# Optimization experiments

Hardware: AMD Instinct MI355X
Metric: run time of the kernel (lower is better)

Reference implementation:

```python
import jax, jax.numpy as jnp
import numpy as np

FEA, DK, H = 512, 64, 8
B, L = 4, 2048
EPS = 1e-5


def _layernorm(x, g, b):
    mu = jnp.mean(x, axis=-1, keepdims=True)
    var = jnp.mean(jnp.square(x - mu), axis=-1, keepdims=True)
    return (x - mu) * jax.lax.rsqrt(var + EPS) * g + b


def setup_inputs() -> dict:
    key = jax.random.key(0)
    ks = jax.random.split(key, 12)
    d = {
        'qx': jax.random.normal(ks[0], (B, L, FEA), jnp.float32),
        'kx': jax.random.normal(ks[1], (B, L, FEA), jnp.float32),
        'vx': jax.random.normal(ks[2], (B, L, FEA), jnp.float32),
        'maskPAD': jax.random.randint(ks[3], (B, L, L), 0, 2, jnp.int32),
        # attention projections (stored as [in, out]); biases zero-init as in module
        'wq': jax.random.normal(ks[4], (FEA, DK * H), jnp.float32) * 0.02,
        'bq': jnp.zeros((DK * H,), jnp.float32),
        'wk': jax.random.normal(ks[5], (FEA, DK * H), jnp.float32) * 0.02,
        'bk': jnp.zeros((DK * H,), jnp.float32),
        'wv': jax.random.normal(ks[6], (FEA, DK * H), jnp.float32) * 0.02,
        'bv': jnp.zeros((DK * H,), jnp.float32),
        'wo': jax.random.normal(ks[7], (DK * H, FEA), jnp.float32) * 0.02,
        'bo': jnp.zeros((FEA,), jnp.float32),
        # FFN
        'w1': jax.random.normal(ks[8], (FEA, 4 * FEA), jnp.float32) * 0.02,
        'b1': jnp.zeros((4 * FEA,), jnp.float32),
        'w2': jax.random.normal(ks[9], (4 * FEA, FEA), jnp.float32) * 0.02,
        'b2': jnp.zeros((FEA,), jnp.float32),
        # layer norms
        'ln1_g': jnp.ones((FEA,), jnp.float32),
        'ln1_b': jnp.zeros((FEA,), jnp.float32),
        'ln2_g': jnp.ones((FEA,), jnp.float32),
        'ln2_b': jnp.zeros((FEA,), jnp.float32),
    }
    return d


def reference(qx, kx, vx, maskPAD, wq, bq, wk, bk, wv, bv, wo, bo,
              w1, b1, w2, b2, ln1_g, ln1_b, ln2_g, ln2_b):
    b, l, _ = qx.shape
    # project and split heads: [B, H, L, DK]
    q = (qx @ wq + bq).reshape(b, l, H, DK).transpose(0, 2, 1, 3)
    k = (kx @ wk + bk).reshape(b, l, H, DK).transpose(0, 2, 1, 3)
    v = (vx @ wv + bv).reshape(b, l, H, DK).transpose(0, 2, 1, 3)
    scores = jnp.einsum('bhqd,bhkd->bhqk', q, k) / np.sqrt(DK)  # [B,H,L,L]
    mask = (maskPAD == 0)[:, None, :, :]
    scores = jnp.where(mask, jnp.float32(-2 ** 15 + 1), scores)
    alpha = jax.nn.softmax(scores, axis=-1)
    z = jnp.einsum('bhqk,bhkd->bhqd', alpha, v)  # [B,H,L,DK]
    z = z.transpose(0, 2, 1, 3).reshape(b, l, H * DK)
    z = z @ wo + bo
    # post-LN FFN block (dropout = identity at inference)
    zn = _layernorm(vx + z, ln1_g, ln1_b)
    ffn = jax.nn.gelu(zn @ w1 + b1, approximate=False) @ w2 + b2
    return _layernorm(zn + ffn, ln2_g, ln2_b)
```

## Files before the change

kernel.cpp:

```cpp
#include <hip/hip_runtime.h>
#include <cstdint>


typedef __bf16 bf16;
typedef __bf16 bf16x8 __attribute__((ext_vector_type(8)));
typedef __bf16 bf16x2 __attribute__((ext_vector_type(2)));
typedef float floatx4 __attribute__((ext_vector_type(4)));
typedef unsigned uint2v __attribute__((ext_vector_type(2)));

__device__ __forceinline__ floatx4 mfma_bf16(bf16x8 a, bf16x8 b, floatx4 c) {
  return __builtin_amdgcn_mfma_f32_16x16x32_bf16(a, b, c, 0, 0, 0);
}

__device__ __forceinline__ void load_lds_16(const void* g, void* l) {
  auto gp = reinterpret_cast<const void __attribute__((address_space(1)))*>(
      reinterpret_cast<uintptr_t>(g));
  auto lp = reinterpret_cast<void __attribute__((address_space(3)))*>(
      (unsigned int)reinterpret_cast<uintptr_t>(l));
  __builtin_amdgcn_global_load_lds(gp, lp, 16, 0, 0);
}

__device__ __forceinline__ unsigned pack2(float a, float b) {
  bf16x2 p;
  p[0] = (bf16)a;
  p[1] = (bf16)b;
  return __builtin_bit_cast(unsigned, p);
}

__device__ __forceinline__ float gelu_f(float x) {
  float t = 0.7978845608f * (x + 0.044715f * x * x * x);
  float e = __builtin_amdgcn_exp2f(t * 2.885390082f);
  float th = 1.0f - 2.0f * __builtin_amdgcn_rcpf(e + 1.0f);
  return 0.5f * x * (1.0f + th);
}

#define PLANE128 2064
#define PLANE64 1040

__global__ void __launch_bounds__(256) transpose4_k(const float* __restrict__ w0,
                                                    const float* __restrict__ w1,
                                                    const float* __restrict__ w2,
                                                    const float* __restrict__ w3,
                                                    bf16* __restrict__ o0,
                                                    bf16* __restrict__ o1,
                                                    bf16* __restrict__ o2,
                                                    bf16* __restrict__ o3) {
  const float* in = (blockIdx.z == 0) ? w0 : (blockIdx.z == 1) ? w1
                    : (blockIdx.z == 2) ? w2 : w3;
  bf16* out = (blockIdx.z == 0) ? o0 : (blockIdx.z == 1) ? o1
              : (blockIdx.z == 2) ? o2 : o3;
  __shared__ float tile[32][33];
  int m0 = blockIdx.x * 32, k0 = blockIdx.y * 32;
  int tx = threadIdx.x, ty = threadIdx.y;
  for (int i = ty; i < 32; i += 8)
    tile[i][tx] = in[(size_t)(k0 + i) * 512 + m0 + tx];
  __syncthreads();
  for (int i = ty; i < 32; i += 8)
    out[(size_t)(m0 + i) * 512 + k0 + tx] = (bf16)tile[tx][i];
}

__global__ void __launch_bounds__(256) transpose_k(const float* __restrict__ in,
                                                   bf16* __restrict__ out,
                                                   int K, int M) {
  __shared__ float tile[32][33];
  int m0 = blockIdx.x * 32, k0 = blockIdx.y * 32;
  int tx = threadIdx.x, ty = threadIdx.y;
  for (int i = ty; i < 32; i += 8)
    tile[i][tx] = in[(size_t)(k0 + i) * M + m0 + tx];
  __syncthreads();
  for (int i = ty; i < 32; i += 8)
    out[(size_t)(m0 + i) * K + k0 + tx] = (bf16)tile[tx][i];
}

__global__ void __launch_bounds__(256) maskbits_k(const int* __restrict__ m,
                                                  unsigned long long* __restrict__ out) {
  int w = blockIdx.x * 4 + (threadIdx.x >> 6);
  int lane = threadIdx.x & 63;
  int v = m[(size_t)w * 64 + lane];
  unsigned long long b = __ballot(v != 0);
  if (lane == 0) out[w] = b;
}

template <int EPI>
__device__ __forceinline__ void epi_store(void* Cout, int n, int m, int M,
                                          float val) {
  if constexpr (EPI == 1) {
    int bb = n >> 11, l = n & 2047, hh = m >> 6, d = m & 63;
    ((bf16*)Cout)[((size_t)((bb * 8 + hh) * 2048 + l)) * 64 + d] = (bf16)val;
  } else if constexpr (EPI == 2) {
    int bb = n >> 11, l = n & 2047, hh = m >> 6, d = m & 63;
    ((bf16*)Cout)[((size_t)((bb * 8 + hh) * 64 + d)) * 2048 + l] = (bf16)val;
  } else if constexpr (EPI == 3) {
    ((bf16*)Cout)[(size_t)n * M + m] = (bf16)gelu_f(val);
  } else if constexpr (EPI == 4) {
    ((float*)Cout)[(size_t)n * M + m] = val;
  } else {
    ((float*)Cout)[(size_t)n * M + m] += val;
  }
}

template <int EPI, bool TALL>
__global__ void __launch_bounds__(256) gemm_bt(const bf16* __restrict__ A,
                                               const bf16* __restrict__ Bt,
                                               const float* __restrict__ bias,
                                               void* __restrict__ Cout,
                                               int M, int K, int lda, int ldb) {
  __shared__ __attribute__((aligned(16))) char As[8 * PLANE128];
  __shared__ __attribute__((aligned(16))) char Bs[TALL ? 8 * PLANE64 : 8 * PLANE128];
  int tid = threadIdx.x, wave = tid >> 6, lane = tid & 63;
  int lrow = lane & 15, quad = lane >> 4;
  int n0 = blockIdx.y * 128;
  int m0 = blockIdx.x * (TALL ? 64 : 128);
  int wr = wave >> 1, wc = wave & 1;
  floatx4 zero4 = {0.f, 0.f, 0.f, 0.f};
  constexpr int NI = TALL ? 2 : 4;
  floatx4 acc[NI][4];
#pragma unroll
  for (int i = 0; i < NI; ++i)
#pragma unroll
    for (int j = 0; j < 4; ++j) acc[i][j] = zero4;
  for (int k0 = 0; k0 < K; k0 += 64) {
    __syncthreads();
#pragma unroll
    for (int h = 0; h < 2; ++h) {
      int p = wave + 4 * h;
#pragma unroll
      for (int j = 0; j < 2; ++j) {
        int row = j * 64 + lane;
        load_lds_16(A + (size_t)(n0 + row) * lda + k0 + p * 8,
                    As + p * PLANE128 + j * 1024 + lane * 16);
      }
      if constexpr (TALL) {
        load_lds_16(Bt + (size_t)(m0 + lane) * ldb + k0 + p * 8,
                    Bs + p * PLANE64 + lane * 16);
      } else {
#pragma unroll
        for (int j = 0; j < 2; ++j) {
          int row = j * 64 + lane;
          load_lds_16(Bt + (size_t)(m0 + row) * ldb + k0 + p * 8,
                      Bs + p * PLANE128 + j * 1024 + lane * 16);
        }
      }
    }
    __syncthreads();
#pragma unroll
    for (int h = 0; h < 2; ++h) {
      int pb = h * 4 + quad;
      bf16x8 af[NI], bfr[4];
#pragma unroll
      for (int i = 0; i < NI; ++i) {
        int row = (TALL ? wave * 32 : wr * 64) + i * 16 + lrow;
        af[i] = *(const bf16x8*)(As + pb * PLANE128 + row * 16);
      }
#pragma unroll
      for (int j = 0; j < 4; ++j) {
        if constexpr (TALL)
          bfr[j] = *(const bf16x8*)(Bs + pb * PLANE64 + (j * 16 + lrow) * 16);
        else
          bfr[j] = *(const bf16x8*)(Bs + pb * PLANE128 +
                                    (wc * 64 + j * 16 + lrow) * 16);
      }
#pragma unroll
      for (int i = 0; i < NI; ++i)
#pragma unroll
        for (int j = 0; j < 4; ++j)
          acc[i][j] = mfma_bf16(af[i], bfr[j], acc[i][j]);
    }
  }
  float bv[4];
#pragma unroll
  for (int j = 0; j < 4; ++j) {
    int m = m0 + (TALL ? 0 : wc * 64) + j * 16 + lrow;
    bv[j] = (EPI == 5) ? 0.f : bias[m];
  }
#pragma unroll
  for (int i = 0; i < NI; ++i)
#pragma unroll
    for (int j = 0; j < 4; ++j)
#pragma unroll
      for (int r = 0; r < 4; ++r) {
        int n = n0 + (TALL ? wave * 32 : wr * 64) + i * 16 + quad * 4 + r;
        int m = m0 + (TALL ? 0 : wc * 64) + j * 16 + lrow;
        epi_store<EPI>(Cout, n, m, M, acc[i][j][r] + bv[j]);
      }
}

__global__ void __launch_bounds__(256) qkv_k(const float* __restrict__ qx,
                                             const float* __restrict__ kx,
                                             const float* __restrict__ vx,
                                             const bf16* __restrict__ wqT,
                                             const bf16* __restrict__ wkT,
                                             const bf16* __restrict__ wvT,
                                             const float* __restrict__ bq,
                                             const float* __restrict__ bk,
                                             const float* __restrict__ bv_,
                                             bf16* __restrict__ qh,
                                             bf16* __restrict__ kh,
                                             bf16* __restrict__ vt) {
  __shared__ __attribute__((aligned(16))) char As[8 * PLANE128];
  __shared__ __attribute__((aligned(16))) char Bs[8 * PLANE128];
  int tid = threadIdx.x, wave = tid >> 6, lane = tid & 63;
  int lrow = lane & 15, quad = lane >> 4;
  int seg = blockIdx.y >> 6;
  int n0 = (blockIdx.y & 63) * 128, m0 = blockIdx.x * 128;
  const float* Af = (seg == 0) ? qx : (seg == 1) ? kx : vx;
  const bf16* Bt = (seg == 0) ? wqT : (seg == 1) ? wkT : wvT;
  const float* bias = (seg == 0) ? bq : (seg == 1) ? bk : bv_;
  bf16* out = (seg == 0) ? qh : (seg == 1) ? kh : vt;
  int wr = wave >> 1, wc = wave & 1;
  floatx4 zero4 = {0.f, 0.f, 0.f, 0.f};
  floatx4 acc[4][4];
#pragma unroll
  for (int i = 0; i < 4; ++i)
#pragma unroll
    for (int j = 0; j < 4; ++j) acc[i][j] = zero4;
  int arow = tid >> 2, ap = tid & 3;
  for (int k0 = 0; k0 < 512; k0 += 64) {
    bf16x8 a[4];
#pragma unroll
    for (int u = 0; u < 4; ++u) {
      int row = arow + (u & 1) * 64, p = ap + (u >> 1) * 4;
      const float* src = Af + (size_t)(n0 + row) * 512 + k0 + p * 8;
      float4 x0 = *(const float4*)src;
      float4 x1 = *(const float4*)(src + 4);
      a[u][0] = (bf16)x0.x; a[u][1] = (bf16)x0.y; a[u][2] = (bf16)x0.z;
      a[u][3] = (bf16)x0.w; a[u][4] = (bf16)x1.x; a[u][5] = (bf16)x1.y;
      a[u][6] = (bf16)x1.z; a[u][7] = (bf16)x1.w;
    }
    __syncthreads();
#pragma unroll
    for (int u = 0; u < 4; ++u) {
      int row = arow + (u & 1) * 64, p = ap + (u >> 1) * 4;
      *(bf16x8*)(As + p * PLANE128 + row * 16) = a[u];
    }
#pragma unroll
    for (int h = 0; h < 2; ++h) {
      int p = wave + 4 * h;
#pragma unroll
      for (int j = 0; j < 2; ++j) {
        int row = j * 64 + lane;
        load_lds_16(Bt + (size_t)(m0 + row) * 512 + k0 + p * 8,
                    Bs + p * PLANE128 + j * 1024 + lane * 16);
      }
    }
    __syncthreads();
#pragma unroll
    for (int h = 0; h < 2; ++h) {
      int pb = h * 4 + quad;
      bf16x8 af[4], bfr[4];
#pragma unroll
      for (int t = 0; t < 4; ++t) {
        af[t] = *(const bf16x8*)(As + pb * PLANE128 + (wr * 64 + t * 16 + lrow) * 16);
        bfr[t] = *(const bf16x8*)(Bs + pb * PLANE128 + (wc * 64 + t * 16 + lrow) * 16);
      }
#pragma unroll
      for (int i = 0; i < 4; ++i)
#pragma unroll
        for (int j = 0; j < 4; ++j) acc[i][j] = mfma_bf16(af[i], bfr[j], acc[i][j]);
    }
  }
  float bvv[4];
#pragma unroll
  for (int j = 0; j < 4; ++j) bvv[j] = bias[m0 + wc * 64 + j * 16 + lrow];
#pragma unroll
  for (int i = 0; i < 4; ++i)
#pragma unroll
    for (int j = 0; j < 4; ++j)
#pragma unroll
      for (int r = 0; r < 4; ++r) {
        int n = n0 + wr * 64 + i * 16 + quad * 4 + r;
        int m = m0 + wc * 64 + j * 16 + lrow;
        float val = acc[i][j][r] + bvv[j];
        int bb = n >> 11, l = n & 2047, hh = m >> 6, d = m & 63;
        if (seg == 2)
          out[((size_t)((bb * 8 + hh) * 64 + d)) * 2048 + l] = (bf16)val;
        else
          out[((size_t)((bb * 8 + hh) * 2048 + l)) * 64 + d] = (bf16)val;
      }
}

__global__ void __launch_bounds__(256) attn_k(const bf16* __restrict__ Qh,
                                              const bf16* __restrict__ Kh,
                                              const bf16* __restrict__ Vt,
                                              const unsigned long long* __restrict__ MB,
                                              bf16* __restrict__ Z) {
  __shared__ __attribute__((aligned(16))) char Ks[2][8 * PLANE64];
  __shared__ __attribute__((aligned(16))) char Vs[2][8 * PLANE64];
  int qt = blockIdx.x, h = blockIdx.y, b = blockIdx.z;
  int tid = threadIdx.x, wave = tid >> 6, lane = tid & 63;
  int lrow = lane & 15, quad = lane >> 4;
  int q0 = qt * 128;
  size_t headbase = (size_t)(b * 8 + h) * 2048 * 64;

  bf16x8 qf[2][2];
#pragma unroll
  for (int u = 0; u < 2; ++u) {
    const bf16* Qp =
        Qh + headbase + (size_t)(q0 + wave * 32 + u * 16 + lrow) * 64 + quad * 8;
    qf[u][0] = *(const bf16x8*)Qp;
    qf[u][1] = *(const bf16x8*)(Qp + 32);
  }

  floatx4 zero4 = {0.f, 0.f, 0.f, 0.f};
  floatx4 o_acc[2][4], acc_l[2];
#pragma unroll
  for (int u = 0; u < 2; ++u) {
    acc_l[u] = zero4;
#pragma unroll
    for (int dt = 0; dt < 4; ++dt) o_acc[u][dt] = zero4;
  }
  bf16x8 ones;
#pragma unroll
  for (int j = 0; j < 8; ++j) ones[j] = (bf16)1.0f;

  const bf16* Vg = Vt + headbase;
  const bf16* Kg0 = Kh + headbase;
  const uint2* MB0 =
      (const uint2*)(MB + ((size_t)b * 2048 + q0 + wave * 32 + lrow) * 32);
  const float C = 0.1803368801f;
  int sh = quad * 4;

  auto stage = [&](int buf, int kt) {
    int kk = kt * 64;
    const bf16* Kg = Kg0 + (size_t)kk * 64;
#pragma unroll
    for (int j = 0; j < 2; ++j) {
      int p = wave * 2 + j;
      load_lds_16(Kg + (size_t)lane * 64 + p * 8,
                  Ks[buf] + p * PLANE64 + lane * 16);
      load_lds_16(Vg + (size_t)lane * 2048 + kk + p * 8,
                  Vs[buf] + p * PLANE64 + lane * 16);
    }
  };

  stage(0, 0);
  uint2 mwc[2] = {MB0[0], MB0[512]};

  for (int kt = 0; kt < 32; ++kt) {
    int cur = kt & 1;
    __syncthreads();
    uint2 mwn[2];
    if (kt < 31) {
      stage(cur ^ 1, kt + 1);
      mwn[0] = MB0[kt + 1];
      mwn[1] = MB0[512 + kt + 1];
    }
    const char* Kc = Ks[cur];
    const char* Vc = Vs[cur];
    unsigned S[2][4][2];
#pragma unroll
    for (int nt = 0; nt < 4; ++nt) {
      int R = nt * 16 + lrow;
      bf16x8 k0f = *(const bf16x8*)(Kc + quad * PLANE64 + R * 16);
      bf16x8 k1f = *(const bf16x8*)(Kc + (quad + 4) * PLANE64 + R * 16);
#pragma unroll
      for (int u = 0; u < 2; ++u) {
        floatx4 aa = zero4;
        aa = mfma_bf16(k0f, qf[u][0], aa);
        aa = mfma_bf16(k1f, qf[u][1], aa);
        floatx4 sc = aa * C;
        unsigned wn = ((nt & 2) ? mwc[u].y : mwc[u].x) >> ((nt & 1) * 16 + sh);
        float e[4];
#pragma unroll
        for (int r = 0; r < 4; ++r)
          e[r] = (wn & (1u << r)) ? __builtin_amdgcn_exp2f(sc[r]) : 0.f;
        S[u][nt][0] = pack2(e[0], e[1]);
        S[u][nt][1] = pack2(e[2], e[3]);
      }
    }
    bf16x8 v0[4], v1[4];
#pragma unroll
    for (int dt = 0; dt < 4; ++dt) {
      int R = dt * 16 + lrow;
      v0[dt] = *(const bf16x8*)(Vc + quad * PLANE64 + R * 16);
      v1[dt] = *(const bf16x8*)(Vc + (quad + 4) * PLANE64 + R * 16);
    }
#pragma unroll
    for (int u = 0; u < 2; ++u) {
      union { unsigned w[4]; bf16x8 v; } pf[2];
#pragma unroll
      for (int half = 0; half < 2; ++half)
#pragma unroll
        for (int pr = 0; pr < 2; ++pr) {
          uint2v a = __builtin_amdgcn_permlane32_swap(
              S[u][half * 2][pr], S[u][half * 2 + 1][pr], false, false);
          uint2v c = __builtin_amdgcn_permlane16_swap(a[0], a[1], false, false);
          pf[half].w[pr] = c[0];
          pf[half].w[pr + 2] = c[1];
        }
      bf16x8 pf0 = pf[0].v, pf1 = pf[1].v;
      __builtin_amdgcn_s_setprio(1);
      acc_l[u] = mfma_bf16(pf0, ones, acc_l[u]);
      acc_l[u] = mfma_bf16(pf1, ones, acc_l[u]);
#pragma unroll
      for (int dt = 0; dt < 4; ++dt) {
        o_acc[u][dt] = mfma_bf16(pf0, v0[dt], o_acc[u][dt]);
        o_acc[u][dt] = mfma_bf16(pf1, v1[dt], o_acc[u][dt]);
      }
      __builtin_amdgcn_s_setprio(0);
    }
    if (kt < 31) { mwc[0] = mwn[0]; mwc[1] = mwn[1]; }
  }
#pragma unroll
  for (int u = 0; u < 2; ++u) {
    float lr[4];
#pragma unroll
    for (int r = 0; r < 4; ++r) lr[r] = 1.0f / acc_l[u][r];
#pragma unroll
    for (int dt = 0; dt < 4; ++dt)
#pragma unroll
      for (int r = 0; r < 4; ++r) {
        int qrow = q0 + wave * 32 + u * 16 + quad * 4 + r;
        int d = dt * 16 + lrow;
        Z[((size_t)(b * 2048 + qrow)) * 512 + h * 64 + d] =
            (bf16)(o_acc[u][dt][r] * lr[r]);
      }
  }
}

template <bool A_BF16, bool OUT_BF16>
__global__ void __launch_bounds__(256) ln_k(const void* __restrict__ a_,
                                            const float* __restrict__ s,
                                            const float* __restrict__ g,
                                            const float* __restrict__ bta,
                                            void* __restrict__ out_) {
  int row = blockIdx.x * 4 + (threadIdx.x >> 6);
  int lane = threadIdx.x & 63;
  size_t base = (size_t)row * 512 + lane * 8;
  float x[8];
  float4 sa = *(const float4*)(s + base);
  float4 sb = *(const float4*)(s + base + 4);
  if constexpr (A_BF16) {
    bf16x8 av = *(const bf16x8*)((const bf16*)a_ + base);
    x[0] = (float)av[0] + sa.x; x[1] = (float)av[1] + sa.y;
    x[2] = (float)av[2] + sa.z; x[3] = (float)av[3] + sa.w;
    x[4] = (float)av[4] + sb.x; x[5] = (float)av[5] + sb.y;
    x[6] = (float)av[6] + sb.z; x[7] = (float)av[7] + sb.w;
  } else {
    float4 a0 = *(const float4*)((const float*)a_ + base);
    float4 a1 = *(const float4*)((const float*)a_ + base + 4);
    x[0] = a0.x + sa.x; x[1] = a0.y + sa.y; x[2] = a0.z + sa.z; x[3] = a0.w + sa.w;
    x[4] = a1.x + sb.x; x[5] = a1.y + sb.y; x[6] = a1.z + sb.z; x[7] = a1.w + sb.w;
  }
  float sum = 0.f;
#pragma unroll
  for (int i = 0; i < 8; ++i) sum += x[i];
#pragma unroll
  for (int off = 1; off < 64; off <<= 1) sum += __shfl_xor(sum, off, 64);
  float mu = sum * (1.0f / 512.0f);
  float vs = 0.f;
#pragma unroll
  for (int i = 0; i < 8; ++i) { float d = x[i] - mu; vs += d * d; }
#pragma unroll
  for (int off = 1; off < 64; off <<= 1) vs += __shfl_xor(vs, off, 64);
  float rstd = rsqrtf(vs * (1.0f / 512.0f) + 1e-5f);
  float4 g0 = *(const float4*)(g + lane * 8);
  float4 g1 = *(const float4*)(g + lane * 8 + 4);
  float4 b0 = *(const float4*)(bta + lane * 8);
  float4 b1 = *(const float4*)(bta + lane * 8 + 4);
  float gg[8] = {g0.x, g0.y, g0.z, g0.w, g1.x, g1.y, g1.z, g1.w};
  float bb[8] = {b0.x, b0.y, b0.z, b0.w, b1.x, b1.y, b1.z, b1.w};
  if constexpr (OUT_BF16) {
    bf16x8 o;
#pragma unroll
    for (int i = 0; i < 8; ++i)
      o[i] = (bf16)((x[i] - mu) * rstd * gg[i] + bb[i]);
    *(bf16x8*)((bf16*)out_ + base) = o;
  } else {
    float4 o0, o1;
    o0.x = (x[0] - mu) * rstd * gg[0] + bb[0];
    o0.y = (x[1] - mu) * rstd * gg[1] + bb[1];
    o0.z = (x[2] - mu) * rstd * gg[2] + bb[2];
    o0.w = (x[3] - mu) * rstd * gg[3] + bb[3];
    o1.x = (x[4] - mu) * rstd * gg[4] + bb[4];
    o1.y = (x[5] - mu) * rstd * gg[5] + bb[5];
    o1.z = (x[6] - mu) * rstd * gg[6] + bb[6];
    o1.w = (x[7] - mu) * rstd * gg[7] + bb[7];
    *(float4*)((float*)out_ + base) = o0;
    *(float4*)((float*)out_ + base + 4) = o1;
  }
}

extern "C" void kernel_launch(void* const* d_in, const int* in_sizes, int n_in,
                              void* d_out, int out_size, void* d_ws, size_t ws_size,
                              hipStream_t stream) {
  const float* qx = (const float*)d_in[0];
  const float* kx = (const float*)d_in[1];
  const float* vx = (const float*)d_in[2];
  const int* maskPAD = (const int*)d_in[3];
  const float* wq = (const float*)d_in[4];
  const float* bq = (const float*)d_in[5];
  const float* wk = (const float*)d_in[6];
  const float* bk = (const float*)d_in[7];
  const float* wv = (const float*)d_in[8];
  const float* bv = (const float*)d_in[9];
  const float* wo = (const float*)d_in[10];
  const float* bo = (const float*)d_in[11];
  const float* w1 = (const float*)d_in[12];
  const float* b1 = (const float*)d_in[13];
  const float* w2 = (const float*)d_in[14];
  const float* b2 = (const float*)d_in[15];
  const float* g1 = (const float*)d_in[16];
  const float* be1 = (const float*)d_in[17];
  const float* g2 = (const float*)d_in[18];
  const float* be2 = (const float*)d_in[19];

  char* w = (char*)d_ws;
  size_t off = 0;
  auto alloc = [&](size_t bytes) {
    void* p = w + off;
    off += (bytes + 255) & ~(size_t)255;
    return p;
  };
  bf16* wqT = (bf16*)alloc(512 * 512 * 2);
  bf16* wkT = (bf16*)alloc(512 * 512 * 2);
  bf16* wvT = (bf16*)alloc(512 * 512 * 2);
  bf16* woT = (bf16*)alloc(512 * 512 * 2);
  bf16* w1T = (bf16*)alloc(2048 * 512 * 2);
  bf16* w2T = (bf16*)alloc(512 * 2048 * 2);
  unsigned long long* mbits = (unsigned long long*)alloc((size_t)4 * 2048 * 32 * 8);
  bf16* qh = (bf16*)alloc((size_t)8192 * 512 * 2);
  bf16* kh = (bf16*)alloc((size_t)8192 * 512 * 2);
  bf16* vt = (bf16*)alloc((size_t)8192 * 512 * 2);
  bf16* z = (bf16*)alloc((size_t)8192 * 512 * 2);
  float* s12 = (float*)qh;
  bf16* zn = vt;
  size_t h1_bytes = (size_t)8192 * 2048 * 2;
  bool big = (off + h1_bytes) <= ws_size;
  bf16* h1 = big ? (bf16*)alloc(h1_bytes) : z;

  dim3 tb(32, 8);
  transpose4_k<<<dim3(16, 16, 4), tb, 0, stream>>>(wq, wk, wv, wo, wqT, wkT, wvT, woT);
  transpose_k<<<dim3(64, 16), tb, 0, stream>>>(w1, w1T, 512, 2048);
  transpose_k<<<dim3(16, 64), tb, 0, stream>>>(w2, w2T, 2048, 512);
  maskbits_k<<<65536, 256, 0, stream>>>(maskPAD, mbits);
  qkv_k<<<dim3(4, 192), 256, 0, stream>>>(qx, kx, vx, wqT, wkT, wvT, bq, bk, bv,
                                          qh, kh, vt);
  attn_k<<<dim3(16, 8, 4), 256, 0, stream>>>(qh, kh, vt, mbits, z);
  gemm_bt<4, true><<<dim3(8, 64), 256, 0, stream>>>(z, woT, bo, s12, 512, 512,
                                                    512, 512);
  ln_k<false, true><<<2048, 256, 0, stream>>>(vx, s12, g1, be1, zn);
  if (big) {
    gemm_bt<3, false><<<dim3(16, 64), 256, 0, stream>>>(zn, w1T, b1, h1, 2048,
                                                        512, 512, 512);
    gemm_bt<4, true><<<dim3(8, 64), 256, 0, stream>>>(h1, w2T, b2, s12, 512,
                                                      2048, 2048, 2048);
  } else {
    for (int p = 0; p < 4; ++p) {
      gemm_bt<3, true><<<dim3(8, 64), 256, 0, stream>>>(
          zn, w1T + (size_t)p * 512 * 512, b1 + p * 512, h1, 512, 512, 512, 512);
      if (p == 0)
        gemm_bt<4, true><<<dim3(8, 64), 256, 0, stream>>>(
            h1, w2T + p * 512, b2, s12, 512, 512, 512, 2048);
      else
        gemm_bt<5, true><<<dim3(8, 64), 256, 0, stream>>>(
            h1, w2T + p * 512, nullptr, s12, 512, 512, 512, 2048);
    }
  }
  ln_k<true, false><<<2048, 256, 0, stream>>>(zn, s12, g2, be2, (float*)d_out);
}
```

Before: 433.2 us.

## Split attention KV range across two wave groups and fold Q scale into projection

The attention kernel now runs 512 threads per block. Two groups of four waves each process half of the key/value tiles with their own double-buffered LDS, and their partial output and row-sum accumulators are combined through LDS at the end. This doubles the waves per block (512 blocks total) to raise occupancy and latency hiding on the attention stage. The softmax scale is moved into the Q projection epilogue, which removes a per-score multiply, at the cost of bf16 rounding of the scaled Q. It also adds an extra reduction with barriers.

```diff
diff --git a/kernel.cpp b/kernel.cpp
--- a/kernel.cpp
+++ b/kernel.cpp
@@ -36,6 +36,7 @@
 
 #define PLANE128 2064
 #define PLANE64 1040
+#define KVCH 8320
 
 __global__ void __launch_bounds__(256) transpose4_k(const float* __restrict__ w0,
                                                     const float* __restrict__ w1,
@@ -262,6 +263,7 @@
   float bvv[4];
 #pragma unroll
   for (int j = 0; j < 4; ++j) bvv[j] = bias[m0 + wc * 64 + j * 16 + lrow];
+  const float qscale = 0.1803368801f;
 #pragma unroll
   for (int i = 0; i < 4; ++i)
 #pragma unroll
@@ -271,6 +273,7 @@
         int n = n0 + wr * 64 + i * 16 + quad * 4 + r;
         int m = m0 + wc * 64 + j * 16 + lrow;
         float val = acc[i][j][r] + bvv[j];
+        if (seg == 0) val *= qscale;
         int bb = n >> 11, l = n & 2047, hh = m >> 6, d = m & 63;
         if (seg == 2)
           out[((size_t)((bb * 8 + hh) * 64 + d)) * 2048 + l] = (bf16)val;
@@ -279,15 +282,15 @@
       }
 }
 
-__global__ void __launch_bounds__(256) attn_k(const bf16* __restrict__ Qh,
-                                              const bf16* __restrict__ Kh,
-                                              const bf16* __restrict__ Vt,
-                                              const unsigned long long* __restrict__ MB,
-                                              bf16* __restrict__ Z) {
-  __shared__ __attribute__((aligned(16))) char Ks[2][8 * PLANE64];
-  __shared__ __attribute__((aligned(16))) char Vs[2][8 * PLANE64];
+__global__ void __launch_bounds__(512, 4) attn_k(const bf16* __restrict__ Qh,
+                                                 const bf16* __restrict__ Kh,
+                                                 const bf16* __restrict__ Vt,
+                                                 const unsigned long long* __restrict__ MB,
+                                                 bf16* __restrict__ Z) {
+  __shared__ __attribute__((aligned(16))) char smem[8 * KVCH];
   int qt = blockIdx.x, h = blockIdx.y, b = blockIdx.z;
   int tid = threadIdx.x, wave = tid >> 6, lane = tid & 63;
+  int hw = wave >> 2, wl = wave & 3;
   int lrow = lane & 15, quad = lane >> 4;
   int q0 = qt * 128;
   size_t headbase = (size_t)(b * 8 + h) * 2048 * 64;
@@ -296,7 +299,7 @@
 #pragma unroll
   for (int u = 0; u < 2; ++u) {
     const bf16* Qp =
-        Qh + headbase + (size_t)(q0 + wave * 32 + u * 16 + lrow) * 64 + quad * 8;
+        Qh + headbase + (size_t)(q0 + wl * 32 + u * 16 + lrow) * 64 + quad * 8;
     qf[u][0] = *(const bf16x8*)Qp;
     qf[u][1] = *(const bf16x8*)(Qp + 32);
   }
@@ -316,37 +319,41 @@
   const bf16* Vg = Vt + headbase;
   const bf16* Kg0 = Kh + headbase;
   const uint2* MB0 =
-      (const uint2*)(MB + ((size_t)b * 2048 + q0 + wave * 32 + lrow) * 32);
-  const float C = 0.1803368801f;
+      (const uint2*)(MB + ((size_t)b * 2048 + q0 + wl * 32 + lrow) * 32);
   int sh = quad * 4;
+
+  char* KsH = smem + hw * 2 * KVCH;
+  char* VsH = smem + 4 * KVCH + hw * 2 * KVCH;
 
   auto stage = [&](int buf, int kt) {
     int kk = kt * 64;
     const bf16* Kg = Kg0 + (size_t)kk * 64;
 #pragma unroll
     for (int j = 0; j < 2; ++j) {
-      int p = wave * 2 + j;
+      int p = wl * 2 + j;
       load_lds_16(Kg + (size_t)lane * 64 + p * 8,
-                  Ks[buf] + p * PLANE64 + lane * 16);
+                  KsH + buf * KVCH + p * PLANE64 + lane * 16);
       load_lds_16(Vg + (size_t)lane * 2048 + kk + p * 8,
-                  Vs[buf] + p * PLANE64 + lane * 16);
+                  VsH + buf * KVCH + p * PLANE64 + lane * 16);
     }
   };
 
-  stage(0, 0);
-  uint2 mwc[2] = {MB0[0], MB0[512]};
-
-  for (int kt = 0; kt < 32; ++kt) {
-    int cur = kt & 1;
+  int ktbase = hw * 16;
+  stage(0, ktbase);
+  uint2 mwc[2] = {MB0[ktbase], MB0[512 + ktbase]};
+
+  for (int it = 0; it < 16; ++it) {
+    int kt = ktbase + it;
+    int cur = it & 1;
     __syncthreads();
     uint2 mwn[2];
-    if (kt < 31) {
+    if (it < 15) {
       stage(cur ^ 1, kt + 1);
       mwn[0] = MB0[kt + 1];
       mwn[1] = MB0[512 + kt + 1];
     }
-    const char* Kc = Ks[cur];
-    const char* Vc = Vs[cur];
+    const char* Kc = KsH + cur * KVCH;
+    const char* Vc = VsH + cur * KVCH;
     unsigned S[2][4][2];
 #pragma unroll
     for (int nt = 0; nt < 4; ++nt) {
@@ -358,12 +365,11 @@
         floatx4 aa = zero4;
         aa = mfma_bf16(k0f, qf[u][0], aa);
         aa = mfma_bf16(k1f, qf[u][1], aa);
-        floatx4 sc = aa * C;
         unsigned wn = ((nt & 2) ? mwc[u].y : mwc[u].x) >> ((nt & 1) * 16 + sh);
         float e[4];
 #pragma unroll
         for (int r = 0; r < 4; ++r)
-          e[r] = (wn & (1u << r)) ? __builtin_amdgcn_exp2f(sc[r]) : 0.f;
+          e[r] = (wn & (1u << r)) ? __builtin_amdgcn_exp2f(aa[r]) : 0.f;
         S[u][nt][0] = pack2(e[0], e[1]);
         S[u][nt][1] = pack2(e[2], e[3]);
       }
@@ -399,22 +405,45 @@
       }
       __builtin_amdgcn_s_setprio(0);
     }
-    if (kt < 31) { mwc[0] = mwn[0]; mwc[1] = mwn[1]; }
-  }
-#pragma unroll
-  for (int u = 0; u < 2; ++u) {
-    float lr[4];
-#pragma unroll
-    for (int r = 0; r < 4; ++r) lr[r] = 1.0f / acc_l[u][r];
-#pragma unroll
-    for (int dt = 0; dt < 4; ++dt)
-#pragma unroll
-      for (int r = 0; r < 4; ++r) {
-        int qrow = q0 + wave * 32 + u * 16 + quad * 4 + r;
-        int d = dt * 16 + lrow;
-        Z[((size_t)(b * 2048 + qrow)) * 512 + h * 64 + d] =
-            (bf16)(o_acc[u][dt][r] * lr[r]);
-      }
+    if (it < 15) { mwc[0] = mwn[0]; mwc[1] = mwn[1]; }
+  }
+
+  __syncthreads();
+  float* cb = (float*)smem;
+  int cbase = (wl * 64 + lane) * 40;
+  if (hw == 1) {
+#pragma unroll
+    for (int u = 0; u < 2; ++u) {
+#pragma unroll
+      for (int dt = 0; dt < 4; ++dt)
+        *(floatx4*)(cb + cbase + (u * 4 + dt) * 4) = o_acc[u][dt];
+      *(floatx4*)(cb + cbase + 32 + u * 4) = acc_l[u];
+    }
+  }
+  __syncthreads();
+  if (hw == 0) {
+#pragma unroll
+    for (int u = 0; u < 2; ++u) {
+#pragma unroll
+      for (int dt = 0; dt < 4; ++dt)
+        o_acc[u][dt] += *(const floatx4*)(cb + cbase + (u * 4 + dt) * 4);
+      acc_l[u] += *(const floatx4*)(cb + cbase + 32 + u * 4);
+    }
+#pragma unroll
+    for (int u = 0; u < 2; ++u) {
+      float lr[4];
+#pragma unroll
+      for (int r = 0; r < 4; ++r) lr[r] = 1.0f / acc_l[u][r];
+#pragma unroll
+      for (int dt = 0; dt < 4; ++dt)
+#pragma unroll
+        for (int r = 0; r < 4; ++r) {
+          int qrow = q0 + wl * 32 + u * 16 + quad * 4 + r;
+          int d = dt * 16 + lrow;
+          Z[((size_t)(b * 2048 + qrow)) * 512 + h * 64 + d] =
+              (bf16)(o_acc[u][dt][r] * lr[r]);
+        }
+    }
   }
 }
 
@@ -536,7 +565,7 @@
   maskbits_k<<<65536, 256, 0, stream>>>(maskPAD, mbits);
   qkv_k<<<dim3(4, 192), 256, 0, stream>>>(qx, kx, vx, wqT, wkT, wvT, bq, bk, bv,
                                           qh, kh, vt);
-  attn_k<<<dim3(16, 8, 4), 256, 0, stream>>>(qh, kh, vt, mbits, z);
+  attn_k<<<dim3(16, 8, 4), 512, 0, stream>>>(qh, kh, vt, mbits, z);
   gemm_bt<4, true><<<dim3(8, 64), 256, 0, stream>>>(z, woT, bo, s12, 512, 512,
                                                     512, 512);
   ln_k<false, true><<<2048, 256, 0, stream>>>(vx, s12, g1, be1, zn);
```

New measurement: 433.3 us. Within noise of the previous version (+0.0%).
